# Kernel tuning notes

Measured on AMD Instinct MI355X. Metric: run time of the kernel, lower is better.

## Reference

```python
import jax, jax.numpy as jnp
import numpy as np

B, C, H, W = 4, 64, 256, 256
HEADS = 4
EPS_LN = 1e-5


def conv2d(x, w, pad, groups=1):
    # x: [B,Cin,H,W], w: [Cout,Cin//groups,kh,kw]
    return jax.lax.conv_general_dilated(
        x, w, window_strides=(1, 1), padding=[(pad, pad), (pad, pad)],
        feature_group_count=groups,
        dimension_numbers=('NCHW', 'OIHW', 'NCHW'))


def layernorm_c(x, w, b):
    # WithBias LayerNorm over channel dim (torch does to_3d -> LN over c -> to_4d)
    mu = jnp.mean(x, axis=1, keepdims=True)
    var = jnp.var(x, axis=1, keepdims=True)
    xn = (x - mu) / jnp.sqrt(var + EPS_LN)
    return xn * w[None, :, None, None] + b[None, :, None, None]


def l2norm(t):
    # torch F.normalize over last dim, eps=1e-12
    n = jnp.linalg.norm(t, axis=-1, keepdims=True)
    return t / jnp.maximum(n, 1e-12)


def setup_inputs() -> dict:
    key = jax.random.key(0)
    ks = jax.random.split(key, 20)
    rn = lambda k, shape, s=0.05: (jax.random.normal(k, shape, jnp.float32) * s)
    return {
        'x':   jax.random.normal(ks[0], (B, C, H, W), jnp.float32),
        'ref': jax.random.normal(ks[1], (B, C, H, W), jnp.float32),
        # LayerNorm params (WithBias)
        'ln1_w': jnp.ones((C,), jnp.float32), 'ln1_b': jnp.zeros((C,), jnp.float32),
        'ln2_w': jnp.ones((C,), jnp.float32), 'ln2_b': jnp.zeros((C,), jnp.float32),
        'ln3_w': jnp.ones((C,), jnp.float32), 'ln3_b': jnp.zeros((C,), jnp.float32),
        # Attention params (bias=False)
        'w_kv':    rn(ks[2], (2 * C, C, 1, 1)),
        'w_kv_dw': rn(ks[3], (2 * C, 1, 3, 3)),
        'w_q':     rn(ks[4], (C, C, 1, 1)),
        'w_q_dw':  rn(ks[5], (C, 1, 3, 3)),
        'w_proj':  rn(ks[6], (C, C, 1, 1)),
        'temperature': jnp.ones((HEADS, 1, 1), jnp.float32),
        # SFM params (bias=False); conv_mul1 is applied twice in the original
        'w_add1': rn(ks[7], (C, C, 3, 3)),
        'w_add2': rn(ks[8], (C, C, 3, 3)),
        'w_mul1': rn(ks[9], (C, C, 3, 3)),
        'w_fuse': rn(ks[10], (C, C, 3, 3)),
    }


def attention(x_kv, x_q, w_kv, w_kv_dw, w_q, w_q_dw, w_proj, temperature):
    b, c, h, w = x_kv.shape
    kv = conv2d(conv2d(x_kv, w_kv, 0), w_kv_dw, 1, groups=2 * c)
    k, v = jnp.split(kv, 2, axis=1)
    q = conv2d(conv2d(x_q, w_q, 0), w_q_dw, 1, groups=c)
    ch = c // HEADS
    resh = lambda t: t.reshape(b, HEADS, ch, h * w)  # b head c (hw)
    q, k, v = l2norm(resh(q)), l2norm(resh(k)), resh(v)
    attn = jnp.einsum('bhcn,bhdn->bhcd', q, k) * temperature[None]  # [b,head,ch,ch]
    attn = jax.nn.softmax(attn, axis=-1)
    out = jnp.einsum('bhcd,bhdn->bhcn', attn, v).reshape(b, c, h, w)
    return conv2d(out, w_proj, 0)


def sfm(x, w_add1, w_add2, w_mul1, w_fuse):
    x_add = conv2d(jax.nn.gelu(conv2d(x, w_add1, 1), approximate=False), w_add2, 1)
    x_mul = conv2d(jax.nn.gelu(conv2d(x, w_mul1, 1), approximate=False), w_mul1, 1)
    x_mul = jax.nn.sigmoid(x_mul)
    return conv2d(x * x_mul + x_add, w_fuse, 1)


def reference(x, ref, ln1_w, ln1_b, ln2_w, ln2_b, ln3_w, ln3_b,
              w_kv, w_kv_dw, w_q, w_q_dw, w_proj, temperature,
              w_add1, w_add2, w_mul1, w_fuse):
    # MyTransformerBlock_FAM.forward(x, ref):
    #   x = x + attn(norm1(ref), norm3(x))  (kv from norm1(ref), q from norm3(x))
    #   x = x + sfm(norm2(x))
    a = attention(layernorm_c(ref, ln1_w, ln1_b), layernorm_c(x, ln3_w, ln3_b),
                  w_kv, w_kv_dw, w_q, w_q_dw, w_proj, temperature)
    x = x + a
    x = x + sfm(layernorm_c(x, ln2_w, ln2_b), w_add1, w_add2, w_mul1, w_fuse)
    return x
```

## Files before the change

### kernel.cpp

```cpp
#include <hip/hip_runtime.h>
#include <math.h>

#define HW 65536
#define NPOS 262144

typedef __attribute__((ext_vector_type(8))) short short8;
typedef __attribute__((ext_vector_type(4))) float float4v;

__device__ __forceinline__ float gelu_exact(float v){
    return 0.5f * v * (1.0f + erff(v * 0.70710678118654752f));
}
__device__ __forceinline__ float sigmoid_(float v){
    return 1.0f / (1.0f + __expf(-v));
}
__device__ __forceinline__ unsigned short f2bf(float f){
    unsigned u = __builtin_bit_cast(unsigned, f);
    unsigned r = (u + 0x7fffu + ((u >> 16) & 1u)) >> 16;
    return (unsigned short)r;
}
__device__ __forceinline__ float bf2f(unsigned short h){
    unsigned u = ((unsigned)h) << 16;
    return __builtin_bit_cast(float, u);
}

__global__ __launch_bounds__(256) void k_wprep(
    const float* __restrict__ w0, const float* __restrict__ w1,
    const float* __restrict__ w2, const float* __restrict__ w3,
    const float* __restrict__ wkv, const float* __restrict__ wq,
    unsigned short* __restrict__ dst,
    unsigned short* __restrict__ whi, unsigned short* __restrict__ wlo)
{
    int gid = blockIdx.x * 256 + threadIdx.x;
    if (gid < 147456){
        int w = gid / 36864;
        int rem = gid - w * 36864;
        int t = rem >> 12;
        int oi = rem & 4095;
        int oc = oi >> 6, ic = oi & 63;
        const float* src = (w == 0) ? w0 : (w == 1) ? w1 : (w == 2) ? w2 : w3;
        dst[gid] = f2bf(src[oc*576 + ic*9 + t]);
    } else {
        int e = gid - 147456;
        int row = e >> 6;
        float f = (row < 128) ? wkv[e] : wq[e - 8192];
        unsigned short h = f2bf(f);
        whi[e] = h;
        wlo[e] = f2bf(f - bf2f(h));
    }
}

__global__ __launch_bounds__(256, 2) void k_ln_1x1_mfma(
    const float* __restrict__ x, const float* __restrict__ ref,
    const float* __restrict__ ln1w, const float* __restrict__ ln1b,
    const float* __restrict__ ln3w, const float* __restrict__ ln3b,
    const unsigned short* __restrict__ whi, const unsigned short* __restrict__ wlo,
    float* __restrict__ kpre, float* __restrict__ vpre, float* __restrict__ qpre,
    float* __restrict__ zbuf)
{
    __shared__ unsigned short Xhi[256*72];
    __shared__ unsigned short Xlo[256*72];
    __shared__ float s_ln[4][64];

    int t = threadIdx.x;
    int b = blockIdx.x >> 8;
    int pos0 = (blockIdx.x & 255) << 8;

    if (blockIdx.x == 0){
        for (int j = t; j < 4608; j += 256) zbuf[j] = 0.f;
    }
    if (t < 64){
        s_ln[0][t] = ln1w[t]; s_ln[1][t] = ln1b[t];
        s_ln[2][t] = ln3w[t]; s_ln[3][t] = ln3b[t];
    }

    int pos = pos0 + t;
    const size_t base = (size_t)b * 64 * HW + pos;
    int wave = t >> 6, lane = t & 63;
    int q = lane >> 4, l = lane & 15;
    int pb = wave * 64;

    {
        float v[64];
        float s = 0.f, ss = 0.f;
        #pragma unroll
        for (int c = 0; c < 64; c++){ float r = ref[base + (size_t)c*HW]; v[c] = r; s += r; ss += r*r; }
        float mu  = s * (1.0f/64.0f);
        float var = ss * (1.0f/64.0f) - mu*mu;
        float inv = rsqrtf(var + 1e-5f);
        __syncthreads();
        #pragma unroll
        for (int c0 = 0; c0 < 64; c0 += 8){
            unsigned short h8[8], l8[8];
            #pragma unroll
            for (int i = 0; i < 8; i++){
                float f = (v[c0+i]-mu)*inv*s_ln[0][c0+i] + s_ln[1][c0+i];
                unsigned short h = f2bf(f);
                h8[i] = h; l8[i] = f2bf(f - bf2f(h));
            }
            *(short8*)(&Xhi[t*72 + c0]) = *(short8*)h8;
            *(short8*)(&Xlo[t*72 + c0]) = *(short8*)l8;
        }
    }
    __syncthreads();

    {
        float4v acc[8][4];
        #pragma unroll
        for (int m = 0; m < 8; m++)
            #pragma unroll
            for (int n = 0; n < 4; n++) acc[m][n] = (float4v){0.f,0.f,0.f,0.f};
        #pragma unroll
        for (int c = 0; c < 2; c++){
            short8 ah[8], al[8];
            #pragma unroll
            for (int m = 0; m < 8; m++){
                ah[m] = *(const short8*)(whi + (m*16 + l)*64 + c*32 + q*8);
                al[m] = *(const short8*)(wlo + (m*16 + l)*64 + c*32 + q*8);
            }
            #pragma unroll
            for (int n = 0; n < 4; n++){
                short8 bh = *(const short8*)(&Xhi[(pb + n*16 + l)*72 + c*32 + q*8]);
                short8 bl = *(const short8*)(&Xlo[(pb + n*16 + l)*72 + c*32 + q*8]);
                #pragma unroll
                for (int m = 0; m < 8; m++){
                    acc[m][n] = __builtin_amdgcn_mfma_f32_16x16x32_bf16(ah[m], bh, acc[m][n], 0, 0, 0);
                    acc[m][n] = __builtin_amdgcn_mfma_f32_16x16x32_bf16(ah[m], bl, acc[m][n], 0, 0, 0);
                    acc[m][n] = __builtin_amdgcn_mfma_f32_16x16x32_bf16(al[m], bh, acc[m][n], 0, 0, 0);
                }
            }
        }
        #pragma unroll
        for (int m = 0; m < 8; m++){
            #pragma unroll
            for (int n = 0; n < 4; n++){
                int px = pos0 + pb + n*16 + l;
                #pragma unroll
                for (int i = 0; i < 4; i++){
                    int oc = m*16 + q*4 + i;
                    float val = acc[m][n][i];
                    if (m < 4) kpre[(size_t)(b*64 + oc)*HW + px] = val;
                    else       vpre[(size_t)(b*64 + (oc-64))*HW + px] = val;
                }
            }
        }
    }
    __syncthreads();

    {
        float v[64];
        float s = 0.f, ss = 0.f;
        #pragma unroll
        for (int c = 0; c < 64; c++){ float r = x[base + (size_t)c*HW]; v[c] = r; s += r; ss += r*r; }
        float mu  = s * (1.0f/64.0f);
        float var = ss * (1.0f/64.0f) - mu*mu;
        float inv = rsqrtf(var + 1e-5f);
        #pragma unroll
        for (int c0 = 0; c0 < 64; c0 += 8){
            unsigned short h8[8], l8[8];
            #pragma unroll
            for (int i = 0; i < 8; i++){
                float f = (v[c0+i]-mu)*inv*s_ln[2][c0+i] + s_ln[3][c0+i];
                unsigned short h = f2bf(f);
                h8[i] = h; l8[i] = f2bf(f - bf2f(h));
            }
            *(short8*)(&Xhi[t*72 + c0]) = *(short8*)h8;
            *(short8*)(&Xlo[t*72 + c0]) = *(short8*)l8;
        }
    }
    __syncthreads();

    {
        float4v acc[4][4];
        #pragma unroll
        for (int m = 0; m < 4; m++)
            #pragma unroll
            for (int n = 0; n < 4; n++) acc[m][n] = (float4v){0.f,0.f,0.f,0.f};
        #pragma unroll
        for (int c = 0; c < 2; c++){
            short8 ah[4], al[4];
            #pragma unroll
            for (int m = 0; m < 4; m++){
                ah[m] = *(const short8*)(whi + (128 + m*16 + l)*64 + c*32 + q*8);
                al[m] = *(const short8*)(wlo + (128 + m*16 + l)*64 + c*32 + q*8);
            }
            #pragma unroll
            for (int n = 0; n < 4; n++){
                short8 bh = *(const short8*)(&Xhi[(pb + n*16 + l)*72 + c*32 + q*8]);
                short8 bl = *(const short8*)(&Xlo[(pb + n*16 + l)*72 + c*32 + q*8]);
                #pragma unroll
                for (int m = 0; m < 4; m++){
                    acc[m][n] = __builtin_amdgcn_mfma_f32_16x16x32_bf16(ah[m], bh, acc[m][n], 0, 0, 0);
                    acc[m][n] = __builtin_amdgcn_mfma_f32_16x16x32_bf16(ah[m], bl, acc[m][n], 0, 0, 0);
                    acc[m][n] = __builtin_amdgcn_mfma_f32_16x16x32_bf16(al[m], bh, acc[m][n], 0, 0, 0);
                }
            }
        }
        #pragma unroll
        for (int m = 0; m < 4; m++){
            #pragma unroll
            for (int n = 0; n < 4; n++){
                int px = pos0 + pb + n*16 + l;
                #pragma unroll
                for (int i = 0; i < 4; i++){
                    int oc = m*16 + q*4 + i;
                    qpre[(size_t)(b*64 + oc)*HW + px] = acc[m][n][i];
                }
            }
        }
    }
}

__global__ __launch_bounds__(256) void k_dw3x3(
    const float* __restrict__ in, const float* __restrict__ w9,
    float* __restrict__ out)
{
    __shared__ float s_in[10*132];
    int t  = threadIdx.x;
    int b  = blockIdx.z >> 6, ch = blockIdx.z & 63;
    int x0 = blockIdx.x * 128, y0 = blockIdx.y * 8;
    const float* src = in + (size_t)(b*64+ch)*HW;
    for (int j = t; j < 1300; j += 256){
        int r = j / 130, cc = j - r*130;
        int gy = y0 - 1 + r, gx = x0 - 1 + cc;
        float val = 0.f;
        if (gy >= 0 && gy < 256 && gx >= 0 && gx < 256) val = src[gy*256 + gx];
        s_in[r*132 + cc] = val;
    }
    float w[9];
    #pragma unroll
    for (int k = 0; k < 9; k++) w[k] = w9[ch*9 + k];
    __syncthreads();
    int ty = t >> 5, tx4 = (t & 31) << 2;
    float o[4] = {0.f, 0.f, 0.f, 0.f};
    #pragma unroll
    for (int ky = 0; ky < 3; ky++){
        float f[6];
        #pragma unroll
        for (int i = 0; i < 6; i++) f[i] = s_in[(ty+ky)*132 + tx4 + i];
        #pragma unroll
        for (int px = 0; px < 4; px++){
            o[px] += w[ky*3+0] * f[px];
            o[px] += w[ky*3+1] * f[px+1];
            o[px] += w[ky*3+2] * f[px+2];
        }
    }
    *(float4v*)(&out[(size_t)(b*64+ch)*HW + (y0+ty)*256 + x0 + tx4]) = *(float4v*)o;
}

__global__ __launch_bounds__(256) void k_qk_mfma(
    const float* __restrict__ q, const float* __restrict__ k,
    float* __restrict__ dots, float* __restrict__ sqq, float* __restrict__ sqk)
{
    int t = threadIdx.x;
    int b = blockIdx.x >> 8;
    int p0 = (blockIdx.x & 255) * 256;
    int wave = t >> 6, lane = t & 63;
    int h = wave;
    int row = lane & 15, kg = lane >> 4;

    const float* qrow = q + (size_t)(b*64 + h*16 + row)*HW;
    const float* krow = k + (size_t)(b*64 + h*16 + row)*HW;

    float4v acc = (float4v){0.f, 0.f, 0.f, 0.f};
    float sq = 0.f, sk = 0.f;

    for (int step = 0; step < 8; step++){
        int p = p0 + step*32 + kg*8;
        float qa[8], ka[8];
        #pragma unroll
        for (int j = 0; j < 8; j++){ qa[j] = qrow[p+j]; ka[j] = krow[p+j]; }
        unsigned short qh8[8], ql8[8], kh8[8], kl8[8];
        #pragma unroll
        for (int j = 0; j < 8; j++){
            sq += qa[j]*qa[j];
            sk += ka[j]*ka[j];
            unsigned short hh = f2bf(qa[j]);
            qh8[j] = hh; ql8[j] = f2bf(qa[j] - bf2f(hh));
            hh = f2bf(ka[j]);
            kh8[j] = hh; kl8[j] = f2bf(ka[j] - bf2f(hh));
        }
        short8 ah = *(short8*)qh8, al = *(short8*)ql8;
        short8 bh = *(short8*)kh8, bl = *(short8*)kl8;
        acc = __builtin_amdgcn_mfma_f32_16x16x32_bf16(ah, bh, acc, 0, 0, 0);
        acc = __builtin_amdgcn_mfma_f32_16x16x32_bf16(ah, bl, acc, 0, 0, 0);
        acc = __builtin_amdgcn_mfma_f32_16x16x32_bf16(al, bh, acc, 0, 0, 0);
    }

    sq += __shfl_xor(sq, 16); sq += __shfl_xor(sq, 32);
    sk += __shfl_xor(sk, 16); sk += __shfl_xor(sk, 32);
    if (lane < 16){
        atomicAdd(&sqq[b*64 + h*16 + row], sq);
        atomicAdd(&sqk[b*64 + h*16 + row], sk);
    }
    int dbase = ((b*4 + h)*16 + kg*4)*16 + row;
    atomicAdd(&dots[dbase + 0*16], acc[0]);
    atomicAdd(&dots[dbase + 1*16], acc[1]);
    atomicAdd(&dots[dbase + 2*16], acc[2]);
    atomicAdd(&dots[dbase + 3*16], acc[3]);
}

__global__ __launch_bounds__(256) void k_softmax_m(
    const float* __restrict__ dots, const float* __restrict__ sqq,
    const float* __restrict__ sqk, const float* __restrict__ temp,
    const float* __restrict__ wproj,
    unsigned short* __restrict__ Mhi, unsigned short* __restrict__ Mlo)
{
    __shared__ float s_wp[4096];
    __shared__ float s_at[1024];
    int t = threadIdx.x;
    int b = blockIdx.x;

    for (int j = t; j < 4096; j += 256) s_wp[j] = wproj[j];

    if (t < 64){
        int h = t >> 4, cq = t & 15;
        float nq = fmaxf(sqrtf(sqq[b*64 + h*16 + cq]), 1e-12f);
        float tp = temp[h];
        float l[16];
        float m = -1e30f;
        #pragma unroll
        for (int d = 0; d < 16; d++){
            float nk = fmaxf(sqrtf(sqk[b*64 + h*16 + d]), 1e-12f);
            float v = dots[((b*4+h)*16 + cq)*16 + d] / (nq*nk) * tp;
            l[d] = v; m = fmaxf(m, v);
        }
        float s = 0.f;
        #pragma unroll
        for (int d = 0; d < 16; d++){ l[d] = __expf(l[d]-m); s += l[d]; }
        float invs = 1.0f / s;
        #pragma unroll
        for (int d = 0; d < 16; d++) s_at[(h*16 + cq)*16 + d] = l[d]*invs;
    }
    __syncthreads();

    for (int e = t; e < 4096; e += 256){
        int c = e >> 6, kk = e & 63;
        int h = kk >> 4, d = kk & 15;
        float a = 0.f;
        #pragma unroll
        for (int r = 0; r < 16; r++)
            a += s_wp[c*64 + h*16 + r] * s_at[(h*16 + r)*16 + d];
        unsigned short hh = f2bf(a);
        Mhi[b*4096 + e] = hh;
        Mlo[b*4096 + e] = f2bf(a - bf2f(hh));
    }
}

__global__ __launch_bounds__(256, 2) void k_attnv_mfma(
    const float* __restrict__ v, const float* __restrict__ x,
    const unsigned short* __restrict__ Mhi_g, const unsigned short* __restrict__ Mlo_g,
    const float* __restrict__ ln2w, const float* __restrict__ ln2b,
    unsigned short* __restrict__ x1_bf, unsigned short* __restrict__ y_bf)
{
    __shared__ unsigned short Mhi[64*72];
    __shared__ unsigned short Mlo[64*72];
    __shared__ float s_lw[64], s_lb[64];
    int t = threadIdx.x;
    int b = blockIdx.x >> 8;
    int pos0 = (blockIdx.x & 255) << 8;

    for (int e = t; e < 4096; e += 256){
        int row = e >> 6, ic = e & 63;
        Mhi[row*72 + ic] = Mhi_g[b*4096 + e];
        Mlo[row*72 + ic] = Mlo_g[b*4096 + e];
    }
    if (t < 64){ s_lw[t] = ln2w[t]; s_lb[t] = ln2b[t]; }
    __syncthreads();

    int wave = t >> 6, lane = t & 63;
    int q = lane >> 4, l = lane & 15;
    int px0 = pos0 + wave*64;

    float4v acc[4][4];
    #pragma unroll
    for (int m = 0; m < 4; m++)
        #pragma unroll
        for (int n = 0; n < 4; n++) acc[m][n] = (float4v){0.f,0.f,0.f,0.f};

    #pragma unroll
    for (int c = 0; c < 2; c++){
        short8 ah[4], al[4];
        #pragma unroll
        for (int m = 0; m < 4; m++){
            ah[m] = *(const short8*)(&Mhi[(m*16 + l)*72 + c*32 + q*8]);
            al[m] = *(const short8*)(&Mlo[(m*16 + l)*72 + c*32 + q*8]);
        }
        #pragma unroll
        for (int n = 0; n < 4; n++){
            float vv[8];
            #pragma unroll
            for (int j = 0; j < 8; j++)
                vv[j] = v[(size_t)(b*64 + c*32 + q*8 + j)*HW + px0 + n*16 + l];
            unsigned short bh8[8], bl8[8];
            #pragma unroll
            for (int j = 0; j < 8; j++){
                unsigned short h = f2bf(vv[j]);
                bh8[j] = h; bl8[j] = f2bf(vv[j] - bf2f(h));
            }
            short8 bh = *(short8*)bh8, bl = *(short8*)bl8;
            #pragma unroll
            for (int m = 0; m < 4; m++){
                acc[m][n] = __builtin_amdgcn_mfma_f32_16x16x32_bf16(ah[m], bh, acc[m][n], 0, 0, 0);
                acc[m][n] = __builtin_amdgcn_mfma_f32_16x16x32_bf16(ah[m], bl, acc[m][n], 0, 0, 0);
                acc[m][n] = __builtin_amdgcn_mfma_f32_16x16x32_bf16(al[m], bh, acc[m][n], 0, 0, 0);
            }
        }
    }

    #pragma unroll
    for (int n = 0; n < 4; n++){
        int px = px0 + n*16 + l;
        float val[4][4];
        float sn = 0.f, ssn = 0.f;
        #pragma unroll
        for (int m = 0; m < 4; m++){
            #pragma unroll
            for (int i = 0; i < 4; i++){
                float f = acc[m][n][i] + x[(size_t)(b*64 + m*16 + q*4 + i)*HW + px];
                val[m][i] = f; sn += f; ssn += f*f;
            }
        }
        sn  += __shfl_xor(sn, 16);  sn  += __shfl_xor(sn, 32);
        ssn += __shfl_xor(ssn, 16); ssn += __shfl_xor(ssn, 32);
        float mu  = sn * (1.0f/64.0f);
        float var = ssn * (1.0f/64.0f) - mu*mu;
        float inv = rsqrtf(var + 1e-5f);
        size_t nb = ((size_t)b*HW + px) * 64;
        #pragma unroll
        for (int m = 0; m < 4; m++){
            int ocb = m*16 + q*4;
            unsigned short xv[4], yv[4];
            #pragma unroll
            for (int i = 0; i < 4; i++){
                float f = val[m][i];
                xv[i] = f2bf(f);
                yv[i] = f2bf((f - mu) * inv * s_lw[ocb+i] + s_lb[ocb+i]);
            }
            *(unsigned long long*)(x1_bf + nb + ocb) = *(unsigned long long*)xv;
            *(unsigned long long*)(y_bf  + nb + ocb) = *(unsigned long long*)yv;
        }
    }
}

__global__ __launch_bounds__(256, 2) void k_conv_dual(
    const unsigned short* __restrict__ in,
    const unsigned short* __restrict__ wtA,
    const unsigned short* __restrict__ wtB,
    unsigned short* __restrict__ o1,
    unsigned short* __restrict__ o2)
{
    __shared__ unsigned short Xs[4*130*40];
    __shared__ unsigned short WsA[2][64*40];
    __shared__ unsigned short WsB[2][64*40];
    int tid  = threadIdx.x;
    int b    = blockIdx.z;
    int y0   = blockIdx.y * 2;
    int x0   = blockIdx.x * 128;
    int wave = tid >> 6, lane = tid & 63;
    int q = lane >> 4, l = lane & 15;
    int r = wave >> 1;
    int pb = (wave & 1) * 64;

    float4v accA[4][4], accB[4][4];
    #pragma unroll
    for (int m = 0; m < 4; m++)
        #pragma unroll
        for (int n = 0; n < 4; n++){
            accA[m][n] = (float4v){0.f,0.f,0.f,0.f};
            accB[m][n] = (float4v){0.f,0.f,0.f,0.f};
        }

    for (int c = 0; c < 2; ++c){
        __syncthreads();
        for (int j = tid; j < 2080; j += 256){
            int row = j / 520;
            int rem = j - row*520;
            int px  = rem >> 2;
            int part= rem & 3;
            int gy = y0 - 1 + row, gx = x0 - 1 + px;
            short8 v = (short8)0;
            if (gy >= 0 && gy < 256 && gx >= 0 && gx < 256){
                v = *(const short8*)(in + (((size_t)b*HW + gy*256 + gx) * 64) + c*32 + part*8);
            }
            *(short8*)(&Xs[(row*130 + px)*40 + part*8]) = v;
        }
        {
            int oc = tid >> 2, part = tid & 3;
            *(short8*)(&WsA[0][oc*40 + part*8]) =
                *(const short8*)(wtA + ((size_t)(0*64 + oc))*64 + c*32 + part*8);
            *(short8*)(&WsB[0][oc*40 + part*8]) =
                *(const short8*)(wtB + ((size_t)(0*64 + oc))*64 + c*32 + part*8);
        }
        for (int t = 0; t < 9; ++t){
            __syncthreads();
            if (t < 8){
                int oc = tid >> 2, part = tid & 3;
                *(short8*)(&WsA[(t+1)&1][oc*40 + part*8]) =
                    *(const short8*)(wtA + ((size_t)((t+1)*64 + oc))*64 + c*32 + part*8);
                *(short8*)(&WsB[(t+1)&1][oc*40 + part*8]) =
                    *(const short8*)(wtB + ((size_t)((t+1)*64 + oc))*64 + c*32 + part*8);
            }
            int ky = t / 3, kx = t - ky*3;
            const unsigned short* wa = &WsA[t & 1][0];
            const unsigned short* wb = &WsB[t & 1][0];
            short8 afrA[4], afrB[4];
            #pragma unroll
            for (int m = 0; m < 4; m++){
                afrA[m] = *(const short8*)(wa + (m*16 + l)*40 + q*8);
                afrB[m] = *(const short8*)(wb + (m*16 + l)*40 + q*8);
            }
            #pragma unroll
            for (int n = 0; n < 4; n++){
                int px = pb + n*16 + l;
                short8 bfr = *(const short8*)(&Xs[((r+ky)*130 + px + kx)*40 + q*8]);
                #pragma unroll
                for (int m = 0; m < 4; m++){
                    accA[m][n] = __builtin_amdgcn_mfma_f32_16x16x32_bf16(afrA[m], bfr, accA[m][n], 0, 0, 0);
                    accB[m][n] = __builtin_amdgcn_mfma_f32_16x16x32_bf16(afrB[m], bfr, accB[m][n], 0, 0, 0);
                }
            }
        }
    }

    int gy = y0 + r;
    #pragma unroll
    for (int n = 0; n < 4; n++){
        int gx = x0 + pb + n*16 + l;
        size_t pixbase = ((size_t)b*HW + gy*256 + gx) * 64;
        #pragma unroll
        for (int m = 0; m < 4; m++){
            int ocb = m*16 + q*4;
            unsigned short p1[4], p2[4];
            #pragma unroll
            for (int i = 0; i < 4; i++){
                p1[i] = f2bf(gelu_exact(accA[m][n][i]));
                p2[i] = f2bf(gelu_exact(accB[m][n][i]));
            }
            *(unsigned long long*)(o1 + pixbase + ocb) = *(unsigned long long*)p1;
            *(unsigned long long*)(o2 + pixbase + ocb) = *(unsigned long long*)p2;
        }
    }
}

__global__ __launch_bounds__(256, 3) void k_conv_zfuse(
    const unsigned short* __restrict__ in1,
    const unsigned short* __restrict__ in2,
    const unsigned short* __restrict__ wtA,
    const unsigned short* __restrict__ wtB,
    const unsigned short* __restrict__ yb,
    unsigned short* __restrict__ zo)
{
    __shared__ unsigned short Xs[4*130*40];
    __shared__ unsigned short Ws[2][64*40];
    int tid  = threadIdx.x;
    int b    = blockIdx.z;
    int y0   = blockIdx.y * 2;
    int x0   = blockIdx.x * 128;
    int wave = tid >> 6, lane = tid & 63;
    int q = lane >> 4, l = lane & 15;
    int r = wave >> 1;
    int pb = (wave & 1) * 64;

    float4v accA[4][4], accB[4][4];
    #pragma unroll
    for (int m = 0; m < 4; m++)
        #pragma unroll
        for (int n = 0; n < 4; n++){
            accA[m][n] = (float4v){0.f,0.f,0.f,0.f};
            accB[m][n] = (float4v){0.f,0.f,0.f,0.f};
        }

    for (int c = 0; c < 2; ++c){
        #pragma unroll
        for (int pass = 0; pass < 2; ++pass){
            const unsigned short* src = (pass == 0) ? in1 : in2;
            const unsigned short* wt  = (pass == 0) ? wtA : wtB;
            __syncthreads();
            for (int j = tid; j < 2080; j += 256){
                int row = j / 520;
                int rem = j - row*520;
                int px  = rem >> 2;
                int part= rem & 3;
                int gy = y0 - 1 + row, gx = x0 - 1 + px;
                short8 v = (short8)0;
                if (gy >= 0 && gy < 256 && gx >= 0 && gx < 256){
                    v = *(const short8*)(src + (((size_t)b*HW + gy*256 + gx) * 64) + c*32 + part*8);
                }
                *(short8*)(&Xs[(row*130 + px)*40 + part*8]) = v;
            }
            {
                int oc = tid >> 2, part = tid & 3;
                *(short8*)(&Ws[0][oc*40 + part*8]) =
                    *(const short8*)(wt + ((size_t)(0*64 + oc))*64 + c*32 + part*8);
            }
            for (int t = 0; t < 9; ++t){
                __syncthreads();
                if (t < 8){
                    int oc = tid >> 2, part = tid & 3;
                    *(short8*)(&Ws[(t+1)&1][oc*40 + part*8]) =
                        *(const short8*)(wt + ((size_t)((t+1)*64 + oc))*64 + c*32 + part*8);
                }
                int ky = t / 3, kx = t - ky*3;
                const unsigned short* wb = &Ws[t & 1][0];
                short8 afr[4];
                #pragma unroll
                for (int m = 0; m < 4; m++)
                    afr[m] = *(const short8*)(wb + (m*16 + l)*40 + q*8);
                #pragma unroll
                for (int n = 0; n < 4; n++){
                    int px = pb + n*16 + l;
                    short8 bfr = *(const short8*)(&Xs[((r+ky)*130 + px + kx)*40 + q*8]);
                    #pragma unroll
                    for (int m = 0; m < 4; m++){
                        if (pass == 0)
                            accA[m][n] = __builtin_amdgcn_mfma_f32_16x16x32_bf16(afr[m], bfr, accA[m][n], 0, 0, 0);
                        else
                            accB[m][n] = __builtin_amdgcn_mfma_f32_16x16x32_bf16(afr[m], bfr, accB[m][n], 0, 0, 0);
                    }
                }
            }
        }
    }

    int gy = y0 + r;
    #pragma unroll
    for (int n = 0; n < 4; n++){
        int gx = x0 + pb + n*16 + l;
        size_t pixbase = ((size_t)b*HW + gy*256 + gx) * 64;
        #pragma unroll
        for (int m = 0; m < 4; m++){
            int ocb = m*16 + q*4;
            unsigned long long yu = *(const unsigned long long*)(yb + pixbase + ocb);
            const unsigned short* y4 = (const unsigned short*)&yu;
            unsigned short pk[4];
            #pragma unroll
            for (int i = 0; i < 4; i++){
                float z = bf2f(y4[i]) * sigmoid_(accB[m][n][i]) + accA[m][n][i];
                pk[i] = f2bf(z);
            }
            *(unsigned long long*)(zo + pixbase + ocb) = *(unsigned long long*)pk;
        }
    }
}

__global__ __launch_bounds__(256, 3) void k_conv_final(
    const unsigned short* __restrict__ in,
    const unsigned short* __restrict__ wt,
    const unsigned short* __restrict__ x1,
    float* __restrict__ outf)
{
    __shared__ unsigned short Xs[4*130*40];
    __shared__ unsigned short Ws[2][64*40];
    int tid  = threadIdx.x;
    int b    = blockIdx.z;
    int y0   = blockIdx.y * 2;
    int x0   = blockIdx.x * 128;
    int wave = tid >> 6, lane = tid & 63;
    int q = lane >> 4, l = lane & 15;
    int r = wave >> 1;
    int pb = (wave & 1) * 64;

    float4v acc[4][4];
    #pragma unroll
    for (int m = 0; m < 4; m++)
        #pragma unroll
        for (int n = 0; n < 4; n++) acc[m][n] = (float4v){0.f,0.f,0.f,0.f};

    for (int c = 0; c < 2; ++c){
        __syncthreads();
        for (int j = tid; j < 2080; j += 256){
            int row = j / 520;
            int rem = j - row*520;
            int px  = rem >> 2;
            int part= rem & 3;
            int gy = y0 - 1 + row, gx = x0 - 1 + px;
            short8 v = (short8)0;
            if (gy >= 0 && gy < 256 && gx >= 0 && gx < 256){
                v = *(const short8*)(in + (((size_t)b*HW + gy*256 + gx) * 64) + c*32 + part*8);
            }
            *(short8*)(&Xs[(row*130 + px)*40 + part*8]) = v;
        }
        {
            int oc = tid >> 2, part = tid & 3;
            *(short8*)(&Ws[0][oc*40 + part*8]) =
                *(const short8*)(wt + ((size_t)(0*64 + oc))*64 + c*32 + part*8);
        }
        for (int t = 0; t < 9; ++t){
            __syncthreads();
            if (t < 8){
                int oc = tid >> 2, part = tid & 3;
                *(short8*)(&Ws[(t+1)&1][oc*40 + part*8]) =
                    *(const short8*)(wt + ((size_t)((t+1)*64 + oc))*64 + c*32 + part*8);
            }
            int ky = t / 3, kx = t - ky*3;
            const unsigned short* wb = &Ws[t & 1][0];
            short8 afr[4];
            #pragma unroll
            for (int m = 0; m < 4; m++)
                afr[m] = *(const short8*)(wb + (m*16 + l)*40 + q*8);
            #pragma unroll
            for (int n = 0; n < 4; n++){
                int px = pb + n*16 + l;
                short8 bfr = *(const short8*)(&Xs[((r+ky)*130 + px + kx)*40 + q*8]);
                #pragma unroll
                for (int m = 0; m < 4; m++)
                    acc[m][n] = __builtin_amdgcn_mfma_f32_16x16x32_bf16(afr[m], bfr, acc[m][n], 0, 0, 0);
            }
        }
    }

    int gy = y0 + r;
    #pragma unroll
    for (int n = 0; n < 4; n++){
        int gx = x0 + pb + n*16 + l;
        size_t pixbase = ((size_t)b*HW + gy*256 + gx) * 64;
        #pragma unroll
        for (int m = 0; m < 4; m++){
            int ocb = m*16 + q*4;
            unsigned long long xu = *(const unsigned long long*)(x1 + pixbase + ocb);
            const unsigned short* x14 = (const unsigned short*)&xu;
            #pragma unroll
            for (int i = 0; i < 4; i++){
                outf[((size_t)(b*64 + ocb + i))*HW + gy*256 + gx] = bf2f(x14[i]) + acc[m][n][i];
            }
        }
    }
}

extern "C" void kernel_launch(void* const* d_in, const int* in_sizes, int n_in,
                              void* d_out, int out_size, void* d_ws, size_t ws_size,
                              hipStream_t stream)
{
    const float* x     = (const float*)d_in[0];
    const float* ref   = (const float*)d_in[1];
    const float* ln1w  = (const float*)d_in[2];
    const float* ln1b  = (const float*)d_in[3];
    const float* ln2w  = (const float*)d_in[4];
    const float* ln2b  = (const float*)d_in[5];
    const float* ln3w  = (const float*)d_in[6];
    const float* ln3b  = (const float*)d_in[7];
    const float* wkv   = (const float*)d_in[8];
    const float* wkvdw = (const float*)d_in[9];
    const float* wq    = (const float*)d_in[10];
    const float* wqdw  = (const float*)d_in[11];
    const float* wproj = (const float*)d_in[12];
    const float* temp  = (const float*)d_in[13];
    const float* wadd1 = (const float*)d_in[14];
    const float* wadd2 = (const float*)d_in[15];
    const float* wmul1 = (const float*)d_in[16];
    const float* wfuse = (const float*)d_in[17];
    float* out = (float*)d_out;

    const size_t S = (size_t)4 * 64 * HW;
    float* ws = (float*)d_ws;
    float* b0   = ws;
    float* b1   = ws + S;
    float* b2   = ws + 2*S;
    float* dots = ws + 3*S;
    float* sqq  = dots + 4096;
    float* sqk  = sqq + 256;
    float* attn = sqk + 256;
    unsigned short* Wt   = (unsigned short*)(attn + 4096);
    unsigned short* Mhi  = Wt + 4*36864;
    unsigned short* Mlo  = Mhi + 4*4096;
    unsigned short* WHhi = Mlo + 4*4096;
    unsigned short* WHlo = WHhi + 12288;
    if (ws_size < 3*S*4 + 8704*4 + (4*36864 + 2*4*4096 + 2*12288)*2) return;

    unsigned short* y_bf  = (unsigned short*)b1;
    unsigned short* x1_bf = (unsigned short*)b1 + S;
    unsigned short* t1_bf = (unsigned short*)b2;
    unsigned short* t2_bf = (unsigned short*)b2 + S;
    unsigned short* z_bf  = (unsigned short*)b0;

    k_wprep<<<624, 256, 0, stream>>>(wadd1, wadd2, wmul1, wfuse, wkv, wq,
                                     Wt, WHhi, WHlo);

    k_ln_1x1_mfma<<<1024, 256, 0, stream>>>(x, ref, ln1w, ln1b, ln3w, ln3b,
                                            WHhi, WHlo, b0, b1, b2, dots);
    dim3 gdw(2, 32, 256);
    k_dw3x3<<<gdw, 256, 0, stream>>>(b2, wqdw,         out);
    k_dw3x3<<<gdw, 256, 0, stream>>>(b0, wkvdw,        b2);
    k_dw3x3<<<gdw, 256, 0, stream>>>(b1, wkvdw + 64*9, b0);

    k_qk_mfma<<<1024, 256, 0, stream>>>(out, b2, dots, sqq, sqk);
    k_softmax_m<<<4, 256, 0, stream>>>(dots, sqq, sqk, temp, wproj, Mhi, Mlo);

    k_attnv_mfma<<<1024, 256, 0, stream>>>(b0, x, Mhi, Mlo, ln2w, ln2b,
                                           x1_bf, y_bf);

    dim3 gc(2, 128, 4);
    k_conv_dual<<<gc, 256, 0, stream>>>(y_bf, Wt + 0*36864, Wt + 2*36864,
                                        t1_bf, t2_bf);
    k_conv_zfuse<<<gc, 256, 0, stream>>>(t1_bf, t2_bf, Wt + 1*36864,
                                         Wt + 2*36864, y_bf, z_bf);
    k_conv_final<<<gc, 256, 0, stream>>>(z_bf, Wt + 3*36864, x1_bf, out);
}
```

Baseline: 680.5 us.

## Prefetch next conv input tile into registers and use LDS-only barriers

Replaces __syncthreads with a custom barrier that waits only on LDS counters, so outstanding global loads no longer stall at every barrier. In the zfuse conv kernel, the next phase's halo tile is loaded into registers while the current phase computes, then written to LDS after the barrier. This adds nine short8 prefetch registers per thread and lowers the occupancy hint from 3 to 2 blocks per CU.

```diff
diff --git a/kernel.cpp b/kernel.cpp
--- a/kernel.cpp
+++ b/kernel.cpp
@@ -21,6 +21,11 @@
 __device__ __forceinline__ float bf2f(unsigned short h){
     unsigned u = ((unsigned)h) << 16;
     return __builtin_bit_cast(float, u);
+}
+
+__device__ __forceinline__ void barrier_lds(){
+    asm volatile("s_waitcnt lgkmcnt(0)" ::: "memory");
+    __builtin_amdgcn_s_barrier();
 }
 
 __global__ __launch_bounds__(256) void k_wprep(
@@ -87,7 +92,7 @@
         float mu  = s * (1.0f/64.0f);
         float var = ss * (1.0f/64.0f) - mu*mu;
         float inv = rsqrtf(var + 1e-5f);
-        __syncthreads();
+        barrier_lds();
         #pragma unroll
         for (int c0 = 0; c0 < 64; c0 += 8){
             unsigned short h8[8], l8[8];
@@ -101,7 +106,7 @@
             *(short8*)(&Xlo[t*72 + c0]) = *(short8*)l8;
         }
     }
-    __syncthreads();
+    barrier_lds();
 
     {
         float4v acc[8][4];
@@ -144,7 +149,7 @@
             }
         }
     }
-    __syncthreads();
+    barrier_lds();
 
     {
         float v[64];
@@ -167,7 +172,7 @@
             *(short8*)(&Xlo[t*72 + c0]) = *(short8*)l8;
         }
     }
-    __syncthreads();
+    barrier_lds();
 
     {
         float4v acc[4][4];
@@ -442,6 +447,42 @@
     }
 }
 
+__device__ __forceinline__ void conv_issue_loads(
+    const unsigned short* __restrict__ src, int b, int y0, int x0, int c,
+    int tid, short8* pf)
+{
+    #pragma unroll
+    for (int u = 0; u < 9; u++){
+        int j = u*256 + tid;
+        if (j < 2080){
+            int row = j / 520;
+            int rem = j - row*520;
+            int px  = rem >> 2;
+            int part= rem & 3;
+            int gy = y0 - 1 + row, gx = x0 - 1 + px;
+            short8 v = (short8)0;
+            if (gy >= 0 && gy < 256 && gx >= 0 && gx < 256)
+                v = *(const short8*)(src + (((size_t)b*HW + gy*256 + gx) * 64) + c*32 + part*8);
+            pf[u] = v;
+        }
+    }
+}
+__device__ __forceinline__ void conv_write_lds(
+    unsigned short* Xs, int tid, const short8* pf)
+{
+    #pragma unroll
+    for (int u = 0; u < 9; u++){
+        int j = u*256 + tid;
+        if (j < 2080){
+            int row = j / 520;
+            int rem = j - row*520;
+            int px  = rem >> 2;
+            int part= rem & 3;
+            *(short8*)(&Xs[(row*130 + px)*40 + part*8]) = pf[u];
+        }
+    }
+}
+
 __global__ __launch_bounds__(256, 2) void k_conv_dual(
     const unsigned short* __restrict__ in,
     const unsigned short* __restrict__ wtA,
@@ -471,7 +512,7 @@
         }
 
     for (int c = 0; c < 2; ++c){
-        __syncthreads();
+        barrier_lds();
         for (int j = tid; j < 2080; j += 256){
             int row = j / 520;
             int rem = j - row*520;
@@ -492,7 +533,7 @@
                 *(const short8*)(wtB + ((size_t)(0*64 + oc))*64 + c*32 + part*8);
         }
         for (int t = 0; t < 9; ++t){
-            __syncthreads();
+            barrier_lds();
             if (t < 8){
                 int oc = tid >> 2, part = tid & 3;
                 *(short8*)(&WsA[(t+1)&1][oc*40 + part*8]) =
@@ -542,7 +583,7 @@
     }
 }
 
-__global__ __launch_bounds__(256, 3) void k_conv_zfuse(
+__global__ __launch_bounds__(256, 2) void k_conv_zfuse(
     const unsigned short* __restrict__ in1,
     const unsigned short* __restrict__ in2,
     const unsigned short* __restrict__ wtA,
@@ -570,53 +611,48 @@
             accB[m][n] = (float4v){0.f,0.f,0.f,0.f};
         }
 
-    for (int c = 0; c < 2; ++c){
-        #pragma unroll
-        for (int pass = 0; pass < 2; ++pass){
-            const unsigned short* src = (pass == 0) ? in1 : in2;
-            const unsigned short* wt  = (pass == 0) ? wtA : wtB;
-            __syncthreads();
-            for (int j = tid; j < 2080; j += 256){
-                int row = j / 520;
-                int rem = j - row*520;
-                int px  = rem >> 2;
-                int part= rem & 3;
-                int gy = y0 - 1 + row, gx = x0 - 1 + px;
-                short8 v = (short8)0;
-                if (gy >= 0 && gy < 256 && gx >= 0 && gx < 256){
-                    v = *(const short8*)(src + (((size_t)b*HW + gy*256 + gx) * 64) + c*32 + part*8);
-                }
-                *(short8*)(&Xs[(row*130 + px)*40 + part*8]) = v;
-            }
-            {
+    short8 pf[9];
+    conv_issue_loads(in1, b, y0, x0, 0, tid, pf);
+
+    #pragma unroll
+    for (int ph = 0; ph < 4; ++ph){
+        const int c    = ph >> 1;
+        const int pass = ph & 1;
+        const unsigned short* wt = (pass == 0) ? wtA : wtB;
+        barrier_lds();
+        conv_write_lds(Xs, tid, pf);
+        {
+            int oc = tid >> 2, part = tid & 3;
+            *(short8*)(&Ws[0][oc*40 + part*8]) =
+                *(const short8*)(wt + ((size_t)oc)*64 + c*32 + part*8);
+        }
+        if (ph < 3){
+            const unsigned short* nsrc = ((ph+1) & 1) ? in2 : in1;
+            conv_issue_loads(nsrc, b, y0, x0, (ph+1) >> 1, tid, pf);
+        }
+        for (int t = 0; t < 9; ++t){
+            barrier_lds();
+            if (t < 8){
                 int oc = tid >> 2, part = tid & 3;
-                *(short8*)(&Ws[0][oc*40 + part*8]) =
-                    *(const short8*)(wt + ((size_t)(0*64 + oc))*64 + c*32 + part*8);
-            }
-            for (int t = 0; t < 9; ++t){
-                __syncthreads();
-                if (t < 8){
-                    int oc = tid >> 2, part = tid & 3;
-                    *(short8*)(&Ws[(t+1)&1][oc*40 + part*8]) =
-                        *(const short8*)(wt + ((size_t)((t+1)*64 + oc))*64 + c*32 + part*8);
-                }
-                int ky = t / 3, kx = t - ky*3;
-                const unsigned short* wb = &Ws[t & 1][0];
-                short8 afr[4];
+                *(short8*)(&Ws[(t+1)&1][oc*40 + part*8]) =
+                    *(const short8*)(wt + ((size_t)((t+1)*64 + oc))*64 + c*32 + part*8);
+            }
+            int ky = t / 3, kx = t - ky*3;
+            const unsigned short* wb = &Ws[t & 1][0];
+            short8 afr[4];
+            #pragma unroll
+            for (int m = 0; m < 4; m++)
+                afr[m] = *(const short8*)(wb + (m*16 + l)*40 + q*8);
+            #pragma unroll
+            for (int n = 0; n < 4; n++){
+                int px = pb + n*16 + l;
+                short8 bfr = *(const short8*)(&Xs[((r+ky)*130 + px + kx)*40 + q*8]);
                 #pragma unroll
-                for (int m = 0; m < 4; m++)
-                    afr[m] = *(const short8*)(wb + (m*16 + l)*40 + q*8);
-                #pragma unroll
-                for (int n = 0; n < 4; n++){
-                    int px = pb + n*16 + l;
-                    short8 bfr = *(const short8*)(&Xs[((r+ky)*130 + px + kx)*40 + q*8]);
-                    #pragma unroll
-                    for (int m = 0; m < 4; m++){
-                        if (pass == 0)
-                            accA[m][n] = __builtin_amdgcn_mfma_f32_16x16x32_bf16(afr[m], bfr, accA[m][n], 0, 0, 0);
-                        else
-                            accB[m][n] = __builtin_amdgcn_mfma_f32_16x16x32_bf16(afr[m], bfr, accB[m][n], 0, 0, 0);
-                    }
+                for (int m = 0; m < 4; m++){
+                    if (pass == 0)
+                        accA[m][n] = __builtin_amdgcn_mfma_f32_16x16x32_bf16(afr[m], bfr, accA[m][n], 0, 0, 0);
+                    else
+                        accB[m][n] = __builtin_amdgcn_mfma_f32_16x16x32_bf16(afr[m], bfr, accB[m][n], 0, 0, 0);
                 }
             }
         }
@@ -667,7 +703,7 @@
         for (int n = 0; n < 4; n++) acc[m][n] = (float4v){0.f,0.f,0.f,0.f};
 
     for (int c = 0; c < 2; ++c){
-        __syncthreads();
+        barrier_lds();
         for (int j = tid; j < 2080; j += 256){
             int row = j / 520;
             int rem = j - row*520;
@@ -686,7 +722,7 @@
                 *(const short8*)(wt + ((size_t)(0*64 + oc))*64 + c*32 + part*8);
         }
         for (int t = 0; t < 9; ++t){
-            __syncthreads();
+            barrier_lds();
             if (t < 8){
                 int oc = tid >> 2, part = tid & 3;
                 *(short8*)(&Ws[(t+1)&1][oc*40 + part*8]) =
```

New measurement: 668.9 us. About the same (-1.7%).
